# Performance work log

Hardware: AMD Instinct MI355X
Metric: run time of the kernel (lower is better)

## Reference

```python
import jax, jax.numpy as jnp
import numpy as np


def conv2d(x, w, b):
    # x: [B,C,H,W], w: [O,I,3,3] 'same' padding, stride 1
    out = jax.lax.conv_general_dilated(
        x, w, window_strides=(1, 1), padding='SAME',
        dimension_numbers=('NCHW', 'OIHW', 'NCHW'))
    return out + b[None, :, None, None]


def gather_for_attn(S, y, u):
    # y: [B,C,H,W], u: [B,S,S] int indices into W -> [B,S*S,H,C]
    B, C, H, W = y.shape
    uu = jnp.clip(u.reshape(B, 1, S * S), 0, W - 1).astype(jnp.int32)
    yf = y.reshape(B, C * H, W)
    g = jnp.take_along_axis(yf, jnp.broadcast_to(uu, (B, C * H, S * S)), axis=2)
    return g.reshape(B, C, H, S * S).transpose(0, 3, 2, 1)


def setup_inputs() -> dict:
    key = jax.random.key(0)
    ks = jax.random.split(key, 12)
    B, C, S = 2, 256, 64
    H, W = 32, 512
    mid, Cz = 128, 128
    sd = 0.05
    inp = {
        'x': jax.random.normal(ks[0], (B, C, S, S), jnp.float32),
        'y': jax.random.normal(ks[1], (B, C, H, W), jnp.float32),
        'z': jax.random.normal(ks[2], (B, Cz, H, W), jnp.float32),
        'u': jax.random.randint(ks[3], (B, S, S), 0, W, jnp.int32),
        'wq1': jax.random.normal(ks[4], (mid, C, 3, 3), jnp.float32) * sd,
        'bq1': jnp.zeros((mid,), jnp.float32),
        'wq2': jax.random.normal(ks[5], (mid, mid, 3, 3), jnp.float32) * sd,
        'bq2': jnp.zeros((mid,), jnp.float32),
        'wk1': jax.random.normal(ks[6], (mid, C, 3, 3), jnp.float32) * sd,
        'bk1': jnp.zeros((mid,), jnp.float32),
        'wk2': jax.random.normal(ks[7], (mid, mid, 3, 3), jnp.float32) * sd,
        'bk2': jnp.zeros((mid,), jnp.float32),
    }
    return inp


def reference(x, y, z, u, wq1, bq1, wq2, bq2, wk1, bk1, wk2, bk2):
    B, C, S, _ = x.shape
    mid = wq1.shape[0]
    scale = mid ** (-0.5)
    # q projection: conv-relu-conv, then flatten spatial -> [B, S*S, mid]
    q = conv2d(jax.nn.relu(conv2d(x, wq1, bq1)), wq2, bq2)
    q = q.reshape(B, mid, S * S).transpose(0, 2, 1)
    # k projection on y, then per-position gather along W -> [B, S*S, H, mid]
    k = conv2d(jax.nn.relu(conv2d(y, wk1, bk1)), wk2, bk2)
    k = gather_for_attn(S, k, u)
    v = gather_for_attn(S, z, u)  # [B, S*S, H, Cz]
    # single query vs H gathered keys; softmax over H
    dot = scale * jnp.einsum('bnc,bnhc->bnh', q, k)
    w = jax.nn.softmax(dot, axis=-1)
    a = jnp.einsum('bnh,bnhc->bnc', w, v)  # [B, S*S, Cz]
    return a
```

## Files before the change

### kernel.cpp

```cpp
#include <hip/hip_runtime.h>


typedef __attribute__((ext_vector_type(8))) _Float16 f16x8;
typedef __attribute__((ext_vector_type(4))) float f32x4;
typedef __attribute__((ext_vector_type(8))) unsigned short us8;
typedef unsigned short u16;

#define MFMA16F(A, B, C) __builtin_amdgcn_mfma_f32_16x16x32_f16((A), (B), (C), 0, 0, 0)


__global__ __launch_bounds__(256) void pack_zero_k(
    const float* __restrict__ wq1, const float* __restrict__ wq2,
    const float* __restrict__ wk1, const float* __restrict__ wk2,
    u16* __restrict__ pq1, u16* __restrict__ pq2,
    u16* __restrict__ pk1, u16* __restrict__ pk2,
    u16* __restrict__ ypad, u16* __restrict__ xpad,
    u16* __restrict__ t2k, u16* __restrict__ t1q)
{
  const int bid = blockIdx.x;
  if (bid < 384) {
    int t = bid * 256 + threadIdx.x;
    const float* w; u16* dst; int IC, tt;
    if (t < 32768)      { w = wq1; dst = pq1; IC = 256; tt = t; }
    else if (t < 49152) { w = wq2; dst = pq2; IC = 128; tt = t - 32768; }
    else if (t < 81920) { w = wk1; dst = pk1; IC = 256; tt = t - 49152; }
    else                { w = wk2; dst = pk2; IC = 128; tt = t - 81920; }
    const int oc = tt / IC, ic = tt % IC;
    const int ICB = IC >> 5;
    const int ocl = oc & 31, ocq = oc >> 5;
    const int swz = ((ocl << 5) | (ic & 31)) ^ ((ocl & 7) << 3);
    #pragma unroll
    for (int rs = 0; rs < 9; ++rs) {
      float v = w[(oc * IC + ic) * 9 + rs];
      long base = (long)rs * (ICB * 4096) + (long)(ic >> 5) * 4096
                + (long)ocq * 1024 + swz;
      dst[base] = __builtin_bit_cast(u16, (_Float16)v);
    }
  } else {
    long u = (long)(bid - 384) * 256 + threadIdx.x;
    if (u >= 32448) return;
    u16* p; int ICB, H, W2;
    if (u < 17472)      { p = ypad; ICB = 8; H = 32; W2 = 514; }
    else if (u < 21632) { u -= 17472; p = xpad; ICB = 8; H = 64; W2 = 66; }
    else if (u < 30368) { u -= 21632; p = t2k; ICB = 4; H = 32; W2 = 514; }
    else                { u -= 30368; p = t1q; ICB = 4; H = 64; W2 = 66; }
    const int H2 = H + 2;
    const long rowsN = (long)2 * ICB * 2 * W2;
    long base;
    if (u < rowsN) {
      int w = (int)(u % W2);
      int t2 = (int)(u / W2);
      int tb = t2 & 1, icb = (t2 >> 1) % ICB, b = (t2 >> 1) / ICB;
      int h = tb ? H2 - 1 : 0;
      base = ((((long)b * H2 + h) * ICB + icb) * W2 + w) * 32;
    } else {
      long v = u - rowsN;
      int side = (int)(v & 1);
      long v2 = v >> 1;
      int h = 1 + (int)(v2 % H);
      int icb = (int)((v2 / H) % ICB);
      int b = (int)(v2 / ((long)H * ICB));
      int w = side ? W2 - 1 : 0;
      base = ((((long)b * H2 + h) * ICB + icb) * W2 + w) * 32;
    }
    us8 zz = {0, 0, 0, 0, 0, 0, 0, 0};
    #pragma unroll
    for (int j = 0; j < 4; ++j)
      *reinterpret_cast<us8*>(&p[base + j * 8]) = zz;
  }
}

__global__ void cvt_all_k(const float* __restrict__ x, const float* __restrict__ y,
                          const float* __restrict__ z,
                          u16* __restrict__ xpad, u16* __restrict__ ypad,
                          u16* __restrict__ zf16)
{
  __shared__ float tile[32][33];
  const int id = blockIdx.x;
  const float* src; int C, H, W, wt, cb, bh, mode, H2, W2;
  u16* d16 = nullptr;
  if (id < 8192)       { src = y; C = 256; H = 32; W = 512; wt = id & 15;       cb = (id >> 4) & 7; bh = id >> 7; d16 = ypad; mode = 0; H2 = 34; W2 = 514; }
  else if (id < 10240) { int i2 = id - 8192;  src = x; C = 256; H = 64; W = 64; wt = i2 & 1;  cb = (i2 >> 1) & 7; bh = i2 >> 4; d16 = xpad; mode = 0; H2 = 66; W2 = 66; }
  else                 { int i3 = id - 10240; src = z; C = 128; H = 32; W = 512; wt = i3 & 15; cb = (i3 >> 4) & 3; bh = i3 >> 6; d16 = zf16; mode = 1; H2 = 0; W2 = 0; }
  const int b = bh / H, h = bh % H;
  const int w0 = wt * 32;
  const int tx = threadIdx.x, ty = threadIdx.y;
  #pragma unroll
  for (int k2 = 0; k2 < 4; ++k2) {
    int c = cb * 32 + ty + k2 * 8;
    tile[ty + k2 * 8][tx] = src[(((long)b * C + c) * H + h) * W + w0 + tx];
  }
  __syncthreads();
  const int j = ty * 32 + tx;
  const int cp = (j & 15) * 2;
  const int wl = j >> 4;
  if (mode == 0) {
    const int ICB = C >> 5;
    #pragma unroll
    for (int half = 0; half < 2; ++half) {
      const int wloc = wl + half * 16;
      unsigned int lo = (unsigned int)__builtin_bit_cast(u16, (_Float16)tile[cp][wloc]);
      unsigned int hi = (unsigned int)__builtin_bit_cast(u16, (_Float16)tile[cp + 1][wloc]);
      long idx = ((((long)b * H2 + h + 1) * ICB + cb) * W2 + (w0 + wloc + 1)) * 32 + cp;
      *reinterpret_cast<unsigned int*>(&d16[idx]) = lo | (hi << 16);
    }
  } else {
    #pragma unroll
    for (int half = 0; half < 2; ++half) {
      const int wloc = wl + half * 16;
      unsigned int lo = (unsigned int)__builtin_bit_cast(u16, (_Float16)tile[cp][wloc]);
      unsigned int hi = (unsigned int)__builtin_bit_cast(u16, (_Float16)tile[cp + 1][wloc]);
      long idx = (((long)b * 32 + h) * 512 + (w0 + wloc)) * 128 + cb * 32 + cp;
      *reinterpret_cast<unsigned int*>(&d16[idx]) = lo | (hi << 16);
    }
  }
}

template<int ICB, int OF16>
__global__ __launch_bounds__(256, 4) void conv_k(
    const u16* __restrict__ inK, const u16* __restrict__ wpkK,
    const float* __restrict__ biasK, u16* __restrict__ outK,
    const u16* __restrict__ inQ, const u16* __restrict__ wpkQ,
    const float* __restrict__ biasQ, u16* __restrict__ outQ)
{
  __shared__ __align__(16) u16 smem[9216];

  const int tid = threadIdx.x;
  const int lane = tid & 63, wv = tid >> 6;
  const int lm = lane & 15, lq = lane >> 4;
  const int bid = blockIdx.x;

  const u16* in; const u16* wpk; const float* bias; u16* outp;
  int IH, IW, PXS, RPB, wpr, w0, hb, rest;
  if (bid < 512) {
    in = inK; wpk = wpkK; bias = biasK; outp = outK;
    IH = 32; IW = 512; PXS = 128; RPB = 2; wpr = 4;
    w0 = (bid & 3) * 128; hb = ((bid >> 2) & 15) * 2; rest = bid >> 6;
  } else {
    int qb = bid - 512;
    in = inQ; wpk = wpkQ; bias = biasQ; outp = outQ;
    IH = 64; IW = 64; PXS = 64; RPB = 4; wpr = 2;
    w0 = 0; hb = (qb & 15) * 4; rest = qb >> 4;
  }
  const int b = rest >> 2, ocq = rest & 3;
  const int H2 = IH + 2, W2 = IW + 2;
  const int rp = wv / wpr, pxw = (wv % wpr) * 32;
  const int hw0 = hb + rp * 2;

  const int aswz0 = (lm * 32 + lq * 8) ^ ((lm & 7) << 3);
  const int aswz1 = aswz0 + 512;

  f32x4 acc[2][2][2];
  #pragma unroll
  for (int mf = 0; mf < 2; ++mf)
    #pragma unroll
    for (int jj = 0; jj < 2; ++jj)
      #pragma unroll
      for (int f = 0; f < 2; ++f) acc[mf][jj][f] = (f32x4)0.f;

  for (int icb = 0; icb < ICB; ++icb) {
    __syncthreads();
    #pragma unroll
    for (int c0 = 0; c0 < 5; ++c0) {
      const int c = c0 * 256 + tid;
      if (c < 1152) {
        const int rs2 = c >> 7;
        const int j = (c & 127) * 8;
        *reinterpret_cast<uint4*>(&smem[rs2 * 1024 + j]) =
            *reinterpret_cast<const uint4*>(
                wpk + (long)rs2 * (ICB * 4096) + (long)icb * 4096 + ocq * 1024 + j);
      }
    }
    const u16* rb[4];
    #pragma unroll
    for (int jr = 0; jr < 4; ++jr)
      rb[jr] = in + ((((long)b * H2 + hw0 + jr) * ICB + icb) * W2 + (w0 + pxw + lm)) * 32
             + lq * 8;
    __syncthreads();

    #pragma unroll
    for (int r = 0; r < 3; ++r)
      #pragma unroll
      for (int s = 0; s < 3; ++s) {
        const int rs = r * 3 + s;
        f16x8 bb[2][2];
        #pragma unroll
        for (int jj = 0; jj < 2; ++jj)
          #pragma unroll
          for (int f = 0; f < 2; ++f)
            bb[jj][f] = *reinterpret_cast<const f16x8*>(rb[jj + r] + (f * 16 + s) * 32);
        const int tb = rs * 1024;
        const f16x8 a0 = *reinterpret_cast<const f16x8*>(&smem[tb + aswz0]);
        const f16x8 a1 = *reinterpret_cast<const f16x8*>(&smem[tb + aswz1]);
        #pragma unroll
        for (int jj = 0; jj < 2; ++jj)
          #pragma unroll
          for (int f = 0; f < 2; ++f) {
            acc[0][jj][f] = MFMA16F(a0, bb[jj][f], acc[0][jj][f]);
            acc[1][jj][f] = MFMA16F(a1, bb[jj][f], acc[1][jj][f]);
          }
      }
  }

  __syncthreads();
  u16* st = smem;
  #pragma unroll
  for (int mf = 0; mf < 2; ++mf)
    #pragma unroll
    for (int jj = 0; jj < 2; ++jj)
      #pragma unroll
      for (int f = 0; f < 2; ++f)
        #pragma unroll
        for (int reg = 0; reg < 4; ++reg) {
          const int ocl = mf * 16 + lq * 4 + reg;
          const int px = pxw + f * 16 + lm;
          const int row = rp * 2 + jj;
          float v = acc[mf][jj][f][reg] + bias[ocq * 32 + ocl];
          if (OF16) v = fmaxf(v, 0.f);
          st[(row * PXS + px) * 32 + (ocl ^ ((px & 3) << 3))] =
              __builtin_bit_cast(u16, (_Float16)v);
        }
  __syncthreads();
  const int tot = RPB * PXS * 4;
  for (int i = tid; i < tot; i += 256) {
    const int o8 = i & 3, pxr = i >> 2;
    const int px = pxr % PXS, row = pxr / PXS;
    us8 val = *reinterpret_cast<const us8*>(
        &st[(row * PXS + px) * 32 + ((o8 * 8) ^ ((px & 3) << 3))]);
    u16* dst;
    if (OF16)
      dst = outp + ((((long)b * H2 + hb + row + 1) * 4 + ocq) * W2 + (w0 + px + 1)) * 32
          + o8 * 8;
    else
      dst = outp + (((long)b * IH + hb + row) * IW + w0 + px) * 128 + ocq * 32 + o8 * 8;
    *reinterpret_cast<us8*>(dst) = val;
  }
}

__global__ __launch_bounds__(128) void attn_k(
    const u16* __restrict__ qf, const u16* __restrict__ kf,
    const u16* __restrict__ zf, const int* __restrict__ u,
    float* __restrict__ out)
{
  constexpr float SCALE = 0.08838834764831845f;
  const int n = blockIdx.x, b = blockIdx.y;
  const int t = threadIdx.x;

  __shared__ float qs[128];
  __shared__ float logit[32];
  __shared__ float el[32];

  int widx = u[b * 4096 + n];
  widx = widx < 0 ? 0 : (widx > 511 ? 511 : widx);

  qs[t] = (float)__builtin_bit_cast(_Float16, qf[((long)b * 4096 + n) * 128 + t]);
  __syncthreads();

  const int h = t >> 2, quad = t & 3;
  const u16* kcol = kf + (((long)b * 32 + h) * 512 + widx) * 128 + quad * 32;
  float p = 0.f;
  #pragma unroll
  for (int j = 0; j < 32; j += 8) {
    f16x8 kv = *reinterpret_cast<const f16x8*>(kcol + j);
    #pragma unroll
    for (int jj = 0; jj < 8; ++jj)
      p = fmaf(qs[quad * 32 + j + jj], (float)kv[jj], p);
  }
  p += __shfl_xor(p, 1);
  p += __shfl_xor(p, 2);
  if (quad == 0) logit[h] = p * SCALE;
  __syncthreads();

  float m = -3.4e38f;
  #pragma unroll
  for (int h2 = 0; h2 < 32; ++h2) m = fmaxf(m, logit[h2]);
  if (t < 32) el[t] = __expf(logit[t] - m);
  __syncthreads();
  float den = 0.f;
  #pragma unroll
  for (int h2 = 0; h2 < 32; ++h2) den += el[h2];

  const u16* zcol = zf + ((long)b * 32 * 512) * 128 + (long)widx * 128 + t;
  float o0 = 0.f, o1 = 0.f, o2 = 0.f, o3 = 0.f;
  #pragma unroll
  for (int h2 = 0; h2 < 32; h2 += 4) {
    o0 = fmaf(el[h2 + 0], (float)__builtin_bit_cast(_Float16, zcol[(long)(h2 + 0) * 512 * 128]), o0);
    o1 = fmaf(el[h2 + 1], (float)__builtin_bit_cast(_Float16, zcol[(long)(h2 + 1) * 512 * 128]), o1);
    o2 = fmaf(el[h2 + 2], (float)__builtin_bit_cast(_Float16, zcol[(long)(h2 + 2) * 512 * 128]), o2);
    o3 = fmaf(el[h2 + 3], (float)__builtin_bit_cast(_Float16, zcol[(long)(h2 + 3) * 512 * 128]), o3);
  }
  out[((long)b * 4096 + n) * 128 + t] = ((o0 + o1) + (o2 + o3)) / den;
}

extern "C" void kernel_launch(void* const* d_in, const int* in_sizes, int n_in,
                              void* d_out, int out_size, void* d_ws, size_t ws_size,
                              hipStream_t stream) {
  const float* x   = (const float*)d_in[0];
  const float* y   = (const float*)d_in[1];
  const float* z   = (const float*)d_in[2];
  const int*   u   = (const int*)  d_in[3];
  const float* wq1 = (const float*)d_in[4];
  const float* bq1 = (const float*)d_in[5];
  const float* wq2 = (const float*)d_in[6];
  const float* bq2 = (const float*)d_in[7];
  const float* wk1 = (const float*)d_in[8];
  const float* bk1 = (const float*)d_in[9];
  const float* wk2 = (const float*)d_in[10];
  const float* bk2 = (const float*)d_in[11];
  float* out = (float*)d_out;
  u16* wsu = (u16*)d_ws;

  u16* ypad  = wsu + 0;
  u16* xpad  = wsu + 8947712;
  u16* t2k   = wsu + 11177984;
  u16* t1q   = wsu + 15651840;
  u16* zf16  = wsu + 16766976;
  u16* k_f16 = wsu + 20961280;
  u16* q_f16 = wsu + 25155584;
  u16* wpk_q1 = wsu + 26204160;
  u16* wpk_q2 = wsu + 26499072;
  u16* wpk_k1 = wsu + 26646528;
  u16* wpk_k2 = wsu + 26941440;

  pack_zero_k<<<dim3(511), 256, 0, stream>>>(wq1, wq2, wk1, wk2,
                                             wpk_q1, wpk_q2, wpk_k1, wpk_k2,
                                             ypad, xpad, t2k, t1q);
  cvt_all_k<<<dim3(14336), dim3(32, 8), 0, stream>>>(x, y, z, xpad, ypad, zf16);
  conv_k<8, 1><<<dim3(640), 256, 0, stream>>>(
      ypad, wpk_k1, bk1, t2k, xpad, wpk_q1, bq1, t1q);
  conv_k<4, 0><<<dim3(640), 256, 0, stream>>>(
      t2k, wpk_k2, bk2, k_f16, t1q, wpk_q2, bq2, q_f16);
  attn_k<<<dim3(4096, 2), 128, 0, stream>>>(q_f16, k_f16, zf16, u, out);
}
```

Before: 112.5 us.

## Load conv weights directly from global memory and merge prep kernels

Weight packing is reordered so each icb block is contiguous per tap, letting the conv kernel read MFMA A-fragments straight from global/L2 instead of staging them through LDS behind two barriers per input-channel block. The separate convert kernel is folded into the pack/zero kernel to save a launch. LDS shrinks and the launch-bounds occupancy hint drops from 4 to 3. In exchange, every wave now issues redundant global weight loads that rely on cache hits, and the removed barrier before the epilogue's smem reuse is safe only because smem is no longer touched in the main loop.

Measured after the change: 126.1 us. +12.1%, slower.

```diff
diff --git a/kernel.cpp b/kernel.cpp
--- a/kernel.cpp
+++ b/kernel.cpp
@@ -9,35 +9,39 @@
 #define MFMA16F(A, B, C) __builtin_amdgcn_mfma_f32_16x16x32_f16((A), (B), (C), 0, 0, 0)
 
 
-__global__ __launch_bounds__(256) void pack_zero_k(
+__global__ __launch_bounds__(256) void prep_k(
+    const float* __restrict__ x, const float* __restrict__ y,
+    const float* __restrict__ z,
     const float* __restrict__ wq1, const float* __restrict__ wq2,
     const float* __restrict__ wk1, const float* __restrict__ wk2,
     u16* __restrict__ pq1, u16* __restrict__ pq2,
     u16* __restrict__ pk1, u16* __restrict__ pk2,
     u16* __restrict__ ypad, u16* __restrict__ xpad,
-    u16* __restrict__ t2k, u16* __restrict__ t1q)
+    u16* __restrict__ t2k, u16* __restrict__ t1q,
+    u16* __restrict__ zf16)
 {
+  __shared__ float tile[32][33];
   const int bid = blockIdx.x;
+  const int tid = threadIdx.x;
+
   if (bid < 384) {
-    int t = bid * 256 + threadIdx.x;
+    int t = bid * 256 + tid;
     const float* w; u16* dst; int IC, tt;
     if (t < 32768)      { w = wq1; dst = pq1; IC = 256; tt = t; }
     else if (t < 49152) { w = wq2; dst = pq2; IC = 128; tt = t - 32768; }
     else if (t < 81920) { w = wk1; dst = pk1; IC = 256; tt = t - 49152; }
     else                { w = wk2; dst = pk2; IC = 128; tt = t - 81920; }
     const int oc = tt / IC, ic = tt % IC;
-    const int ICB = IC >> 5;
     const int ocl = oc & 31, ocq = oc >> 5;
-    const int swz = ((ocl << 5) | (ic & 31)) ^ ((ocl & 7) << 3);
+    const int icb = ic >> 5, icl = ic & 31;
     #pragma unroll
     for (int rs = 0; rs < 9; ++rs) {
       float v = w[(oc * IC + ic) * 9 + rs];
-      long base = (long)rs * (ICB * 4096) + (long)(ic >> 5) * 4096
-                + (long)ocq * 1024 + swz;
+      long base = ((((long)icb * 9 + rs) * 4 + ocq) * 32 + ocl) * 32 + icl;
       dst[base] = __builtin_bit_cast(u16, (_Float16)v);
     }
-  } else {
-    long u = (long)(bid - 384) * 256 + threadIdx.x;
+  } else if (bid < 511) {
+    long u = (long)(bid - 384) * 256 + tid;
     if (u >= 32448) return;
     u16* p; int ICB, H, W2;
     if (u < 17472)      { p = ypad; ICB = 8; H = 32; W2 = 514; }
@@ -67,63 +71,55 @@
     #pragma unroll
     for (int j = 0; j < 4; ++j)
       *reinterpret_cast<us8*>(&p[base + j * 8]) = zz;
+  } else {
+    const int id = bid - 511;
+    const float* src; int C, H, W, wt, cb, bh, mode, H2, W2;
+    u16* d16;
+    if (id < 8192)       { src = y; C = 256; H = 32; W = 512; wt = id & 15;       cb = (id >> 4) & 7; bh = id >> 7; d16 = ypad; mode = 0; H2 = 34; W2 = 514; }
+    else if (id < 10240) { int i2 = id - 8192;  src = x; C = 256; H = 64; W = 64; wt = i2 & 1;  cb = (i2 >> 1) & 7; bh = i2 >> 4; d16 = xpad; mode = 0; H2 = 66; W2 = 66; }
+    else                 { int i3 = id - 10240; src = z; C = 128; H = 32; W = 512; wt = i3 & 15; cb = (i3 >> 4) & 3; bh = i3 >> 6; d16 = zf16; mode = 1; H2 = 0; W2 = 0; }
+    const int b = bh / H, h = bh % H;
+    const int w0 = wt * 32;
+    const int tx = tid & 31, ty = tid >> 5;
+    #pragma unroll
+    for (int k2 = 0; k2 < 4; ++k2) {
+      int c = cb * 32 + ty + k2 * 8;
+      tile[ty + k2 * 8][tx] = src[(((long)b * C + c) * H + h) * W + w0 + tx];
+    }
+    __syncthreads();
+    const int cp = (tid & 15) * 2;
+    const int wl = tid >> 4;
+    if (mode == 0) {
+      const int ICB = C >> 5;
+      #pragma unroll
+      for (int half = 0; half < 2; ++half) {
+        const int wloc = wl + half * 16;
+        unsigned int lo = (unsigned int)__builtin_bit_cast(u16, (_Float16)tile[cp][wloc]);
+        unsigned int hi = (unsigned int)__builtin_bit_cast(u16, (_Float16)tile[cp + 1][wloc]);
+        long idx = ((((long)b * H2 + h + 1) * ICB + cb) * W2 + (w0 + wloc + 1)) * 32 + cp;
+        *reinterpret_cast<unsigned int*>(&d16[idx]) = lo | (hi << 16);
+      }
+    } else {
+      #pragma unroll
+      for (int half = 0; half < 2; ++half) {
+        const int wloc = wl + half * 16;
+        unsigned int lo = (unsigned int)__builtin_bit_cast(u16, (_Float16)tile[cp][wloc]);
+        unsigned int hi = (unsigned int)__builtin_bit_cast(u16, (_Float16)tile[cp + 1][wloc]);
+        long idx = (((long)b * 32 + h) * 512 + (w0 + wloc)) * 128 + cb * 32 + cp;
+        *reinterpret_cast<unsigned int*>(&d16[idx]) = lo | (hi << 16);
+      }
+    }
   }
 }
 
-__global__ void cvt_all_k(const float* __restrict__ x, const float* __restrict__ y,
-                          const float* __restrict__ z,
-                          u16* __restrict__ xpad, u16* __restrict__ ypad,
-                          u16* __restrict__ zf16)
-{
-  __shared__ float tile[32][33];
-  const int id = blockIdx.x;
-  const float* src; int C, H, W, wt, cb, bh, mode, H2, W2;
-  u16* d16 = nullptr;
-  if (id < 8192)       { src = y; C = 256; H = 32; W = 512; wt = id & 15;       cb = (id >> 4) & 7; bh = id >> 7; d16 = ypad; mode = 0; H2 = 34; W2 = 514; }
-  else if (id < 10240) { int i2 = id - 8192;  src = x; C = 256; H = 64; W = 64; wt = i2 & 1;  cb = (i2 >> 1) & 7; bh = i2 >> 4; d16 = xpad; mode = 0; H2 = 66; W2 = 66; }
-  else                 { int i3 = id - 10240; src = z; C = 128; H = 32; W = 512; wt = i3 & 15; cb = (i3 >> 4) & 3; bh = i3 >> 6; d16 = zf16; mode = 1; H2 = 0; W2 = 0; }
-  const int b = bh / H, h = bh % H;
-  const int w0 = wt * 32;
-  const int tx = threadIdx.x, ty = threadIdx.y;
-  #pragma unroll
-  for (int k2 = 0; k2 < 4; ++k2) {
-    int c = cb * 32 + ty + k2 * 8;
-    tile[ty + k2 * 8][tx] = src[(((long)b * C + c) * H + h) * W + w0 + tx];
-  }
-  __syncthreads();
-  const int j = ty * 32 + tx;
-  const int cp = (j & 15) * 2;
-  const int wl = j >> 4;
-  if (mode == 0) {
-    const int ICB = C >> 5;
-    #pragma unroll
-    for (int half = 0; half < 2; ++half) {
-      const int wloc = wl + half * 16;
-      unsigned int lo = (unsigned int)__builtin_bit_cast(u16, (_Float16)tile[cp][wloc]);
-      unsigned int hi = (unsigned int)__builtin_bit_cast(u16, (_Float16)tile[cp + 1][wloc]);
-      long idx = ((((long)b * H2 + h + 1) * ICB + cb) * W2 + (w0 + wloc + 1)) * 32 + cp;
-      *reinterpret_cast<unsigned int*>(&d16[idx]) = lo | (hi << 16);
-    }
-  } else {
-    #pragma unroll
-    for (int half = 0; half < 2; ++half) {
-      const int wloc = wl + half * 16;
-      unsigned int lo = (unsigned int)__builtin_bit_cast(u16, (_Float16)tile[cp][wloc]);
-      unsigned int hi = (unsigned int)__builtin_bit_cast(u16, (_Float16)tile[cp + 1][wloc]);
-      long idx = (((long)b * 32 + h) * 512 + (w0 + wloc)) * 128 + cb * 32 + cp;
-      *reinterpret_cast<unsigned int*>(&d16[idx]) = lo | (hi << 16);
-    }
-  }
-}
-
 template<int ICB, int OF16>
-__global__ __launch_bounds__(256, 4) void conv_k(
+__global__ __launch_bounds__(256, 3) void conv_k(
     const u16* __restrict__ inK, const u16* __restrict__ wpkK,
     const float* __restrict__ biasK, u16* __restrict__ outK,
     const u16* __restrict__ inQ, const u16* __restrict__ wpkQ,
     const float* __restrict__ biasQ, u16* __restrict__ outQ)
 {
-  __shared__ __align__(16) u16 smem[9216];
+  __shared__ __align__(16) u16 smem[8192];
 
   const int tid = threadIdx.x;
   const int lane = tid & 63, wv = tid >> 6;
@@ -147,8 +143,7 @@
   const int rp = wv / wpr, pxw = (wv % wpr) * 32;
   const int hw0 = hb + rp * 2;
 
-  const int aswz0 = (lm * 32 + lq * 8) ^ ((lm & 7) << 3);
-  const int aswz1 = aswz0 + 512;
+  const int alane = (ocq * 32 + lm) * 32 + lq * 8;
 
   f32x4 acc[2][2][2];
   #pragma unroll
@@ -159,24 +154,12 @@
       for (int f = 0; f < 2; ++f) acc[mf][jj][f] = (f32x4)0.f;
 
   for (int icb = 0; icb < ICB; ++icb) {
-    __syncthreads();
-    #pragma unroll
-    for (int c0 = 0; c0 < 5; ++c0) {
-      const int c = c0 * 256 + tid;
-      if (c < 1152) {
-        const int rs2 = c >> 7;
-        const int j = (c & 127) * 8;
-        *reinterpret_cast<uint4*>(&smem[rs2 * 1024 + j]) =
-            *reinterpret_cast<const uint4*>(
-                wpk + (long)rs2 * (ICB * 4096) + (long)icb * 4096 + ocq * 1024 + j);
-      }
-    }
     const u16* rb[4];
     #pragma unroll
     for (int jr = 0; jr < 4; ++jr)
       rb[jr] = in + ((((long)b * H2 + hw0 + jr) * ICB + icb) * W2 + (w0 + pxw + lm)) * 32
              + lq * 8;
-    __syncthreads();
+    const u16* wt = wpk + (long)icb * 9 * 4096 + alane;
 
     #pragma unroll
     for (int r = 0; r < 3; ++r)
@@ -189,9 +172,8 @@
           #pragma unroll
           for (int f = 0; f < 2; ++f)
             bb[jj][f] = *reinterpret_cast<const f16x8*>(rb[jj + r] + (f * 16 + s) * 32);
-        const int tb = rs * 1024;
-        const f16x8 a0 = *reinterpret_cast<const f16x8*>(&smem[tb + aswz0]);
-        const f16x8 a1 = *reinterpret_cast<const f16x8*>(&smem[tb + aswz1]);
+        const f16x8 a0 = *reinterpret_cast<const f16x8*>(wt + rs * 4096);
+        const f16x8 a1 = *reinterpret_cast<const f16x8*>(wt + rs * 4096 + 512);
         #pragma unroll
         for (int jj = 0; jj < 2; ++jj)
           #pragma unroll
@@ -202,7 +184,6 @@
       }
   }
 
-  __syncthreads();
   u16* st = smem;
   #pragma unroll
   for (int mf = 0; mf < 2; ++mf)
@@ -322,10 +303,9 @@
   u16* wpk_k1 = wsu + 26646528;
   u16* wpk_k2 = wsu + 26941440;
 
-  pack_zero_k<<<dim3(511), 256, 0, stream>>>(wq1, wq2, wk1, wk2,
-                                             wpk_q1, wpk_q2, wpk_k1, wpk_k2,
-                                             ypad, xpad, t2k, t1q);
-  cvt_all_k<<<dim3(14336), dim3(32, 8), 0, stream>>>(x, y, z, xpad, ypad, zf16);
+  prep_k<<<dim3(14847), 256, 0, stream>>>(x, y, z, wq1, wq2, wk1, wk2,
+                                          wpk_q1, wpk_q2, wpk_k1, wpk_k2,
+                                          ypad, xpad, t2k, t1q, zf16);
   conv_k<8, 1><<<dim3(640), 256, 0, stream>>>(
       ypad, wpk_k1, bk1, t2k, xpad, wpk_q1, bq1, t1q);
   conv_k<4, 0><<<dim3(640), 256, 0, stream>>>(
```
